# Kernel optimization log

Hardware: AMD Instinct MI355X
Metric: run time of the kernel (lower is better)

## Reference

```python
import jax, jax.numpy as jnp
import numpy as np

HID = 1024
NTOK = 16
BIAS_SCALE = 1.5
EPS = 1e-5


def layer_norm(x, g, b):
    mu = jnp.mean(x, axis=-1, keepdims=True)
    var = jnp.mean(jnp.square(x - mu), axis=-1, keepdims=True)
    return (x - mu) * jax.lax.rsqrt(var + EPS) * g + b


def setup_inputs() -> dict:
    key = jax.random.key(0)
    ks = jax.random.split(key, 16)
    B, T = 8, 4096
    Dt, Ds, Dp = 512, 512, 64
    Din = Dt + Ds + Dp

    def lin(k, fan_in, fan_out):
        bound = 1.0 / np.sqrt(fan_in)
        k1, k2 = jax.random.split(k)
        W = jax.random.uniform(k1, (fan_in, fan_out), jnp.float32, -bound, bound)
        b = jax.random.uniform(k2, (fan_out,), jnp.float32, -bound, bound)
        return W, b

    W_in, b_in = lin(ks[0], Din, HID)
    W_m1, b_m1 = lin(ks[1], HID, HID)
    W_m2, b_m2 = lin(ks[2], HID, HID)
    W_o1, b_o1 = lin(ks[3], HID, HID // 2)
    W_o2, b_o2 = lin(ks[4], HID // 2, 1)
    return {
        "trace_features": jax.random.normal(ks[5], (B, T, Dt), jnp.float32),
        "semantic_features": jax.random.normal(ks[6], (B, T, Ds), jnp.float32),
        "prior_features": jax.random.normal(ks[7], (B, T, Dp), jnp.float32),
        "W_in": W_in, "b_in": b_in,
        "ln_in_g": jnp.ones((HID,), jnp.float32), "ln_in_b": jnp.zeros((HID,), jnp.float32),
        "W_m1": W_m1, "b_m1": b_m1, "W_m2": W_m2, "b_m2": b_m2,
        "W_o1": W_o1, "b_o1": b_o1, "W_o2": W_o2, "b_o2": b_o2,
        "token_queries": jax.random.normal(ks[8], (NTOK, HID), jnp.float32) * 0.02,
        "ln_out_g": jnp.ones((HID,), jnp.float32), "ln_out_b": jnp.zeros((HID,), jnp.float32),
    }


def reference(trace_features, semantic_features, prior_features,
              W_in, b_in, ln_in_g, ln_in_b,
              W_m1, b_m1, W_m2, b_m2,
              W_o1, b_o1, W_o2, b_o2,
              token_queries, ln_out_g, ln_out_b):
    # fuse inputs: [B, T, Dt+Ds+Dp]
    fused = jnp.concatenate([trace_features, semantic_features, prior_features], axis=-1)
    h = fused @ W_in + b_in  # [B, T, H]
    mlp = jax.nn.gelu(h @ W_m1 + b_m1, approximate=False) @ W_m2 + b_m2
    seq_hidden = layer_norm(h + mlp, ln_in_g, ln_in_b)

    # objectness head -> [B, T]
    obj_logits = (jax.nn.gelu(seq_hidden @ W_o1 + b_o1, approximate=False) @ W_o2 + b_o2)[..., 0]
    objectness = jax.nn.sigmoid(obj_logits)

    # learned-query cross attention with objectness bias
    scale = float(HID) ** -0.5
    attn_logits = jnp.einsum('nh,bth->bnt', token_queries, seq_hidden) * scale
    attn_logits = attn_logits + BIAS_SCALE * objectness[:, None, :]
    attn = jax.nn.softmax(attn_logits, axis=-1)  # [B, N, T]
    token_values = jnp.einsum('bnt,bth->bnh', attn, seq_hidden)
    state_tokens = layer_norm(token_queries[None] + token_values, ln_out_g, ln_out_b)
    return state_tokens, attn, objectness
```

## Files before the change

kernel.cpp:

```cpp
#include <hip/hip_runtime.h>
#include <hip/hip_bf16.h>
#include <math.h>

typedef __bf16 bf16;
typedef __bf16 bf16x8 __attribute__((ext_vector_type(8)));
typedef __bf16 bf16x4 __attribute__((ext_vector_type(4)));
typedef float f32x4 __attribute__((ext_vector_type(4)));

#define KM 32768
#define DIN 1088

__device__ __forceinline__ void gload16(const void* g, void* l) {
  __builtin_amdgcn_global_load_lds((const __attribute__((address_space(1))) void*)g,
                                   (__attribute__((address_space(3))) void*)l, 16, 0, 0);
}

__device__ __forceinline__ float gelu_exact(float x) {
  return 0.5f * x * (1.0f + erff(x * 0.70710678118654752f));
}

__global__ void fuse_kernel(const float* __restrict__ tr, const float* __restrict__ se,
                            const float* __restrict__ pr, bf16* __restrict__ Xb) {
  int g = blockIdx.x * 256 + threadIdx.x;
  if (g >= KM * 272) return;
  int m = g / 272;
  int k0 = (g - m * 272) * 4;
  float4 v;
  if (k0 < 512)       v = *reinterpret_cast<const float4*>(tr + (size_t)m * 512 + k0);
  else if (k0 < 1024) v = *reinterpret_cast<const float4*>(se + (size_t)m * 512 + (k0 - 512));
  else                v = *reinterpret_cast<const float4*>(pr + (size_t)m * 64 + (k0 - 1024));
  union { bf16 h[4]; ushort4 u; } p;
  p.h[0] = (bf16)v.x; p.h[1] = (bf16)v.y; p.h[2] = (bf16)v.z; p.h[3] = (bf16)v.w;
  *reinterpret_cast<ushort4*>(Xb + (size_t)m * 1088 + k0) = p.u;
}

__global__ void transpose_kernel(const float* __restrict__ W, bf16* __restrict__ Wt,
                                 int K, int N) {
  __shared__ float t[32][33];
  int k0 = blockIdx.x * 32, n0 = blockIdx.y * 32;
  int tx = threadIdx.x & 31, ty = threadIdx.x >> 5;
  #pragma unroll
  for (int j = 0; j < 32; j += 8) t[ty + j][tx] = W[(size_t)(k0 + ty + j) * N + n0 + tx];
  __syncthreads();
  #pragma unroll
  for (int j = 0; j < 32; j += 8)
    Wt[(size_t)(n0 + ty + j) * K + k0 + tx] = (bf16)t[tx][ty + j];
}

template<int ACT, bool RES>
__global__ void gemm_kernel(const bf16* __restrict__ A, const bf16* __restrict__ Bt,
                            const float* __restrict__ bias, const bf16* __restrict__ res,
                            bf16* __restrict__ C, int N, int K, int nbn) {
  __shared__ __align__(16) bf16 lds[2][128 * 64];
  int bid = blockIdx.x;
  int bn = bid % nbn, bm = bid / nbn;
  int tid = threadIdx.x;
  int w = tid >> 6, L = tid & 63;
  int wm = w >> 1, wn = w & 1;
  int srow = L >> 3;
  int scol = 8 * ((L & 7) ^ srow);
  const bf16* Ab = A + (size_t)(bm * 128) * K;
  const bf16* Bb = Bt + (size_t)(bn * 128) * K;
  f32x4 acc[4][4] = {};
  int nkt = K >> 6;
  for (int kt = 0; kt < nkt; ++kt) {
    int k0 = kt << 6;
    #pragma unroll
    for (int i = 0; i < 4; ++i) {
      int row = w * 32 + i * 8;
      gload16(Ab + (size_t)(row + srow) * K + k0 + scol, &lds[0][row * 64]);
      gload16(Bb + (size_t)(row + srow) * K + k0 + scol, &lds[1][row * 64]);
    }
    __syncthreads();
    #pragma unroll
    for (int kk = 0; kk < 2; ++kk) {
      bf16x8 af[4], bfr[4];
      int cb = kk * 64 + ((L >> 4) * 16);
      #pragma unroll
      for (int m = 0; m < 4; ++m) {
        int r = wm * 64 + m * 16 + (L & 15);
        int addr = r * 128 + (cb ^ ((r & 7) << 4));
        af[m] = *reinterpret_cast<const bf16x8*>(
            reinterpret_cast<const char*>(&lds[0][0]) + addr);
      }
      #pragma unroll
      for (int n = 0; n < 4; ++n) {
        int r = wn * 64 + n * 16 + (L & 15);
        int addr = r * 128 + (cb ^ ((r & 7) << 4));
        bfr[n] = *reinterpret_cast<const bf16x8*>(
            reinterpret_cast<const char*>(&lds[1][0]) + addr);
      }
      #pragma unroll
      for (int m = 0; m < 4; ++m)
        #pragma unroll
        for (int n = 0; n < 4; ++n)
          acc[m][n] = __builtin_amdgcn_mfma_f32_16x16x32_bf16(af[m], bfr[n], acc[m][n], 0, 0, 0);
    }
    __syncthreads();
  }
  int cn0 = bn * 128 + wn * 64;
  float bv[4];
  #pragma unroll
  for (int n = 0; n < 4; ++n) bv[n] = bias[cn0 + n * 16 + (L & 15)];
  #pragma unroll
  for (int m = 0; m < 4; ++m) {
    int grow0 = bm * 128 + wm * 64 + m * 16 + ((L >> 4) << 2);
    #pragma unroll
    for (int r = 0; r < 4; ++r) {
      size_t ro = (size_t)(grow0 + r) * N;
      #pragma unroll
      for (int n = 0; n < 4; ++n) {
        float v = acc[m][n][r] + bv[n];
        if (ACT == 1) v = gelu_exact(v);
        int col = cn0 + n * 16 + (L & 15);
        if (RES) v += (float)res[ro + col];
        C[ro + col] = (bf16)v;
      }
    }
  }
}

__global__ void ln_inplace_kernel(bf16* __restrict__ X, const float* __restrict__ g,
                                  const float* __restrict__ b) {
  __shared__ float sb[4];
  size_t row = blockIdx.x;
  bf16* xr = X + row * 1024;
  int tid = threadIdx.x;
  bf16x4 xv = *reinterpret_cast<const bf16x4*>(xr + tid * 4);
  float x[4];
  #pragma unroll
  for (int i = 0; i < 4; ++i) x[i] = (float)xv[i];
  float s = x[0] + x[1] + x[2] + x[3];
  #pragma unroll
  for (int off = 32; off > 0; off >>= 1) s += __shfl_xor(s, off);
  if ((tid & 63) == 0) sb[tid >> 6] = s;
  __syncthreads();
  float mu = (sb[0] + sb[1] + sb[2] + sb[3]) * (1.0f / 1024.0f);
  __syncthreads();
  float d[4], sq = 0.f;
  #pragma unroll
  for (int i = 0; i < 4; ++i) { d[i] = x[i] - mu; sq += d[i] * d[i]; }
  #pragma unroll
  for (int off = 32; off > 0; off >>= 1) sq += __shfl_xor(sq, off);
  if ((tid & 63) == 0) sb[tid >> 6] = sq;
  __syncthreads();
  float var = (sb[0] + sb[1] + sb[2] + sb[3]) * (1.0f / 1024.0f);
  float rs = rsqrtf(var + 1e-5f);
  bf16x4 ov;
  #pragma unroll
  for (int i = 0; i < 4; ++i) ov[i] = (bf16)(d[i] * rs * g[tid * 4 + i] + b[tid * 4 + i]);
  *reinterpret_cast<bf16x4*>(xr + tid * 4) = ov;
}

__global__ void obj_kernel(const bf16* __restrict__ o1, const float* __restrict__ W2,
                           const float* __restrict__ b2, float* __restrict__ obj,
                           float* __restrict__ out_obj) {
  __shared__ float w[512];
  int tid = threadIdx.x;
  w[tid] = W2[tid]; w[tid + 256] = W2[tid + 256];
  __syncthreads();
  int wv = tid >> 6, L = tid & 63;
  size_t m = (size_t)blockIdx.x * 4 + wv;
  bf16x8 v = *reinterpret_cast<const bf16x8*>(o1 + m * 512 + L * 8);
  float s = 0.f;
  #pragma unroll
  for (int j = 0; j < 8; ++j) s += (float)v[j] * w[L * 8 + j];
  #pragma unroll
  for (int off = 32; off > 0; off >>= 1) s += __shfl_xor(s, off);
  if (L == 0) {
    float o = 1.0f / (1.0f + expf(-(s + b2[0])));
    obj[m] = o; out_obj[m] = o;
  }
}

__global__ void attn_logits_mfma(const bf16* __restrict__ seq, const float* __restrict__ tq,
                                 const float* __restrict__ obj, float* __restrict__ logits) {
  __shared__ bf16 tqs[16][1032];
  int tid = threadIdx.x;
  for (int i = tid; i < 4096; i += 256) {
    int idx = i * 4;
    int n = idx >> 10, k = idx & 1023;
    float4 v = *reinterpret_cast<const float4*>(tq + idx);
    bf16x4 p; p[0] = (bf16)v.x; p[1] = (bf16)v.y; p[2] = (bf16)v.z; p[3] = (bf16)v.w;
    *reinterpret_cast<bf16x4*>(&tqs[n][k]) = p;
  }
  __syncthreads();
  int w = tid >> 6, L = tid & 63;
  int row0 = blockIdx.x * 128 + w * 32;
  const bf16* A0 = seq + (size_t)(row0 + (L & 15)) * 1024 + ((L >> 4) * 8);
  const bf16* Bq = &tqs[L & 15][(L >> 4) * 8];
  f32x4 acc0 = {}, acc1 = {};
  #pragma unroll 4
  for (int kt = 0; kt < 32; ++kt) {
    int k0 = kt * 32;
    bf16x8 bq = *reinterpret_cast<const bf16x8*>(Bq + k0);
    bf16x8 a0 = *reinterpret_cast<const bf16x8*>(A0 + k0);
    bf16x8 a1 = *reinterpret_cast<const bf16x8*>(A0 + 16 * 1024 + k0);
    acc0 = __builtin_amdgcn_mfma_f32_16x16x32_bf16(a0, bq, acc0, 0, 0, 0);
    acc1 = __builtin_amdgcn_mfma_f32_16x16x32_bf16(a1, bq, acc1, 0, 0, 0);
  }
  int b = row0 >> 12;
  int n = L & 15;
  float* outn = logits + ((size_t)(b * 16) + n) * 4096;
  #pragma unroll
  for (int mf = 0; mf < 2; ++mf) {
    int mrow = row0 + mf * 16 + ((L >> 4) << 2);
    #pragma unroll
    for (int r = 0; r < 4; ++r) {
      int m = mrow + r;
      float v = (mf == 0 ? acc0[r] : acc1[r]) * 0.03125f + 1.5f * obj[m];
      outn[m & 4095] = v;
    }
  }
}

__global__ void softmax_kernel(const float* __restrict__ logits, float* __restrict__ attn) {
  __shared__ float sb[4];
  size_t row = blockIdx.x;
  const float* lr = logits + row * 4096;
  float* orow = attn + row * 4096;
  int tid = threadIdx.x;
  float x[16];
  #pragma unroll
  for (int i = 0; i < 4; ++i) {
    float4 v = *reinterpret_cast<const float4*>(lr + tid * 16 + i * 4);
    x[i * 4 + 0] = v.x; x[i * 4 + 1] = v.y; x[i * 4 + 2] = v.z; x[i * 4 + 3] = v.w;
  }
  float mx = -1e30f;
  #pragma unroll
  for (int j = 0; j < 16; ++j) mx = fmaxf(mx, x[j]);
  #pragma unroll
  for (int off = 32; off > 0; off >>= 1) mx = fmaxf(mx, __shfl_xor(mx, off));
  if ((tid & 63) == 0) sb[tid >> 6] = mx;
  __syncthreads();
  mx = fmaxf(fmaxf(sb[0], sb[1]), fmaxf(sb[2], sb[3]));
  __syncthreads();
  float s = 0.f;
  #pragma unroll
  for (int j = 0; j < 16; ++j) { x[j] = expf(x[j] - mx); s += x[j]; }
  #pragma unroll
  for (int off = 32; off > 0; off >>= 1) s += __shfl_xor(s, off);
  if ((tid & 63) == 0) sb[tid >> 6] = s;
  __syncthreads();
  float inv = 1.0f / (sb[0] + sb[1] + sb[2] + sb[3]);
  #pragma unroll
  for (int i = 0; i < 4; ++i) {
    float4 v = make_float4(x[i * 4] * inv, x[i * 4 + 1] * inv, x[i * 4 + 2] * inv, x[i * 4 + 3] * inv);
    *reinterpret_cast<float4*>(orow + tid * 16 + i * 4) = v;
  }
}

__global__ void token_values_kernel(const float* __restrict__ attn, const bf16* __restrict__ seq,
                                    float* __restrict__ tvp) {
  int bid = blockIdx.x;
  int split = bid & 3;
  int hc = (bid >> 2) & 15;
  int b = bid >> 6;
  __shared__ float al[16][256];
  int h = hc * 64 + (threadIdx.x & 63);
  int grp = threadIdx.x >> 6;
  float acc[4] = {0.f, 0.f, 0.f, 0.f};
  for (int c = 0; c < 4; ++c) {
    int t0 = split * 1024 + c * 256;
    __syncthreads();
    for (int i = threadIdx.x; i < 4096; i += 256)
      al[i >> 8][i & 255] = attn[((size_t)b * 16 + (i >> 8)) * 4096 + t0 + (i & 255)];
    __syncthreads();
    for (int tt = 0; tt < 256; ++tt) {
      float s = (float)seq[((size_t)b * 4096 + t0 + tt) * 1024 + h];
      #pragma unroll
      for (int i = 0; i < 4; ++i) acc[i] += al[grp * 4 + i][tt] * s;
    }
  }
  #pragma unroll
  for (int i = 0; i < 4; ++i)
    tvp[(size_t)split * 131072 + ((size_t)b * 16 + grp * 4 + i) * 1024 + h] = acc[i];
}

__global__ void final_ln_kernel(const float* __restrict__ tq, const float* __restrict__ tvp,
                                const float* __restrict__ g, const float* __restrict__ bb,
                                float* __restrict__ out0) {
  __shared__ float sb[4];
  int row = blockIdx.x;
  int n = row & 15;
  int tid = threadIdx.x;
  float x[4];
  #pragma unroll
  for (int i = 0; i < 4; ++i) {
    int h = tid * 4 + i;
    float v = tq[n * 1024 + h];
    #pragma unroll
    for (int p = 0; p < 4; ++p) v += tvp[(size_t)p * 131072 + (size_t)row * 1024 + h];
    x[i] = v;
  }
  float s = x[0] + x[1] + x[2] + x[3];
  #pragma unroll
  for (int off = 32; off > 0; off >>= 1) s += __shfl_xor(s, off);
  if ((tid & 63) == 0) sb[tid >> 6] = s;
  __syncthreads();
  float mu = (sb[0] + sb[1] + sb[2] + sb[3]) * (1.0f / 1024.0f);
  __syncthreads();
  float d[4], sq = 0.f;
  #pragma unroll
  for (int i = 0; i < 4; ++i) { d[i] = x[i] - mu; sq += d[i] * d[i]; }
  #pragma unroll
  for (int off = 32; off > 0; off >>= 1) sq += __shfl_xor(sq, off);
  if ((tid & 63) == 0) sb[tid >> 6] = sq;
  __syncthreads();
  float var = (sb[0] + sb[1] + sb[2] + sb[3]) * (1.0f / 1024.0f);
  float rs = rsqrtf(var + 1e-5f);
  #pragma unroll
  for (int i = 0; i < 4; ++i) {
    int h = tid * 4 + i;
    out0[(size_t)row * 1024 + h] = d[i] * rs * g[h] + bb[h];
  }
}

extern "C" void kernel_launch(void* const* d_in, const int* in_sizes, int n_in,
                              void* d_out, int out_size, void* d_ws, size_t ws_size,
                              hipStream_t stream) {
  const float* tr      = (const float*)d_in[0];
  const float* se      = (const float*)d_in[1];
  const float* pr      = (const float*)d_in[2];
  const float* W_in    = (const float*)d_in[3];
  const float* b_in    = (const float*)d_in[4];
  const float* ln_in_g = (const float*)d_in[5];
  const float* ln_in_b = (const float*)d_in[6];
  const float* W_m1    = (const float*)d_in[7];
  const float* b_m1    = (const float*)d_in[8];
  const float* W_m2    = (const float*)d_in[9];
  const float* b_m2    = (const float*)d_in[10];
  const float* W_o1    = (const float*)d_in[11];
  const float* b_o1    = (const float*)d_in[12];
  const float* W_o2    = (const float*)d_in[13];
  const float* b_o2    = (const float*)d_in[14];
  const float* tq      = (const float*)d_in[15];
  const float* ln_out_g= (const float*)d_in[16];
  const float* ln_out_b= (const float*)d_in[17];

  float* out       = (float*)d_out;
  float* out_state = out;
  float* out_attn  = out + 131072;
  float* out_obj   = out + 131072 + 524288;

  char* ws = (char*)d_ws;
  size_t off = 0;
  auto alloc = [&](size_t bytes) {
    char* p = ws + off;
    off += (bytes + 255) & ~(size_t)255;
    return p;
  };
  bf16*  Xb   = (bf16*)alloc(71303168);
  bf16*  t1   = Xb;
  bf16*  hb   = (bf16*)alloc(67108864);
  bf16*  o1   = hb;
  bf16*  sq   = (bf16*)alloc(67108864);
  bf16*  WbIn = (bf16*)alloc(2228224);
  bf16*  WbM1 = (bf16*)alloc(2097152);
  bf16*  WbM2 = (bf16*)alloc(2097152);
  bf16*  WbO1 = (bf16*)alloc(1048576);
  float* objw = (float*)alloc(131072 * 4);
  float* logw = (float*)alloc(2097152);
  float* tvp  = (float*)alloc(2097152);

  fuse_kernel<<<(KM * 272 + 255) / 256, 256, 0, stream>>>(tr, se, pr, Xb);
  transpose_kernel<<<dim3(34, 32), 256, 0, stream>>>(W_in, WbIn, 1088, 1024);
  transpose_kernel<<<dim3(32, 32), 256, 0, stream>>>(W_m1, WbM1, 1024, 1024);
  transpose_kernel<<<dim3(32, 32), 256, 0, stream>>>(W_m2, WbM2, 1024, 1024);
  transpose_kernel<<<dim3(32, 16), 256, 0, stream>>>(W_o1, WbO1, 1024, 512);

  gemm_kernel<0, false><<<256 * 8, 256, 0, stream>>>(Xb, WbIn, b_in, nullptr, hb, 1024, 1088, 8);
  gemm_kernel<1, false><<<256 * 8, 256, 0, stream>>>(hb, WbM1, b_m1, nullptr, t1, 1024, 1024, 8);
  gemm_kernel<0, true ><<<256 * 8, 256, 0, stream>>>(t1, WbM2, b_m2, hb, sq, 1024, 1024, 8);
  ln_inplace_kernel<<<32768, 256, 0, stream>>>(sq, ln_in_g, ln_in_b);
  gemm_kernel<1, false><<<256 * 4, 256, 0, stream>>>(sq, WbO1, b_o1, nullptr, o1, 512, 1024, 4);
  obj_kernel<<<8192, 256, 0, stream>>>(o1, W_o2, b_o2, objw, out_obj);
  attn_logits_mfma<<<256, 256, 0, stream>>>(sq, tq, objw, logw);
  softmax_kernel<<<128, 256, 0, stream>>>(logw, out_attn);
  token_values_kernel<<<512, 256, 0, stream>>>(out_attn, sq, tvp);
  final_ln_kernel<<<128, 256, 0, stream>>>(tq, tvp, ln_out_g, ln_out_b, out_state);
}
```

Measured before the change: 516.7 us.

## Replace 128x128 GEMM with 256x256 tile, 8-wave pipelined double-buffered kernel

```diff
diff --git a/kernel.cpp b/kernel.cpp
--- a/kernel.cpp
+++ b/kernel.cpp
@@ -9,6 +9,9 @@
 
 #define KM 32768
 #define DIN 1088
+
+#define BAR() asm volatile("s_barrier" ::: "memory")
+#define WAIT_VM2() asm volatile("s_waitcnt vmcnt(2)" ::: "memory")
 
 __device__ __forceinline__ void gload16(const void* g, void* l) {
   __builtin_amdgcn_global_load_lds((const __attribute__((address_space(1))) void*)g,
@@ -48,71 +51,140 @@
 }
 
 template<int ACT, bool RES>
-__global__ void gemm_kernel(const bf16* __restrict__ A, const bf16* __restrict__ Bt,
-                            const float* __restrict__ bias, const bf16* __restrict__ res,
-                            bf16* __restrict__ C, int N, int K, int nbn) {
-  __shared__ __align__(16) bf16 lds[2][128 * 64];
+__global__ __launch_bounds__(512, 2) void gemm256_kernel(
+    const bf16* __restrict__ A, const bf16* __restrict__ Bt,
+    const float* __restrict__ bias, const bf16* __restrict__ res,
+    bf16* __restrict__ C, int N, int K, int nbn) {
+  __shared__ __align__(16) bf16 ldsA[2][16384];
+  __shared__ __align__(16) bf16 ldsB[2][16384];
+  int nwg = gridDim.x;
   int bid = blockIdx.x;
-  int bn = bid % nbn, bm = bid / nbn;
+  int nb = (bid & 7) * (nwg >> 3) + (bid >> 3);
+  int bn = nb % nbn, bm = nb / nbn;
   int tid = threadIdx.x;
   int w = tid >> 6, L = tid & 63;
-  int wm = w >> 1, wn = w & 1;
-  int srow = L >> 3;
-  int scol = 8 * ((L & 7) ^ srow);
-  const bf16* Ab = A + (size_t)(bm * 128) * K;
-  const bf16* Bb = Bt + (size_t)(bn * 128) * K;
-  f32x4 acc[4][4] = {};
+  int wm = w >> 2, wn = w & 3;
+  const bf16* Ab = A + (size_t)bm * 256 * K;
+  const bf16* Bb = Bt + (size_t)bn * 256 * K;
   int nkt = K >> 6;
-  for (int kt = 0; kt < nkt; ++kt) {
-    int k0 = kt << 6;
-    #pragma unroll
-    for (int i = 0; i < 4; ++i) {
-      int row = w * 32 + i * 8;
-      gload16(Ab + (size_t)(row + srow) * K + k0 + scol, &lds[0][row * 64]);
-      gload16(Bb + (size_t)(row + srow) * K + k0 + scol, &lds[1][row * 64]);
+  int H = nkt << 2;
+
+  int lr = L >> 3;
+  int ce = ((L & 7) ^ lr) << 3;
+  auto stage = [&](int h) {
+    if (h >= H) return;
+    int tt = h >> 2, i = h & 3, bb = tt & 1;
+    int k0 = tt << 6;
+    #pragma unroll
+    for (int j = 0; j < 2; ++j) {
+      int rr = w * 16 + j * 8;
+      if (i < 2)
+        gload16(Ab + (size_t)(i * 128 + rr + lr) * K + k0 + ce, &ldsA[bb][(i * 128 + rr) * 64]);
+      else
+        gload16(Bb + (size_t)((i - 2) * 128 + rr + lr) * K + k0 + ce, &ldsB[bb][((i - 2) * 128 + rr) * 64]);
     }
-    __syncthreads();
-    #pragma unroll
-    for (int kk = 0; kk < 2; ++kk) {
-      bf16x8 af[4], bfr[4];
-      int cb = kk * 64 + ((L >> 4) * 16);
-      #pragma unroll
-      for (int m = 0; m < 4; ++m) {
-        int r = wm * 64 + m * 16 + (L & 15);
-        int addr = r * 128 + (cb ^ ((r & 7) << 4));
-        af[m] = *reinterpret_cast<const bf16x8*>(
-            reinterpret_cast<const char*>(&lds[0][0]) + addr);
-      }
-      #pragma unroll
-      for (int n = 0; n < 4; ++n) {
-        int r = wn * 64 + n * 16 + (L & 15);
-        int addr = r * 128 + (cb ^ ((r & 7) << 4));
-        bfr[n] = *reinterpret_cast<const bf16x8*>(
-            reinterpret_cast<const char*>(&lds[1][0]) + addr);
-      }
-      #pragma unroll
-      for (int m = 0; m < 4; ++m)
+  };
+  auto lread = [&](const bf16* base, int mrow, int kk) -> bf16x8 {
+    int cb = ((kk << 6) + ((L >> 4) << 4)) ^ ((L & 7) << 4);
+    return *reinterpret_cast<const bf16x8*>(
+        reinterpret_cast<const char*>(base) + (mrow + (L & 15)) * 128 + cb);
+  };
+
+  f32x4 acc[8][4] = {};
+  bf16x8 af[4][2], bq[4][2];
+
+  #pragma unroll
+  for (int h = 0; h < 5; ++h) stage(h);
+  WAIT_VM2();
+  BAR();
+
+  for (int t = 0; t < nkt; ++t) {
+    int b = t & 1;
+    const bf16* As = ldsA[b];
+    const bf16* Bs = ldsB[b];
+    #pragma unroll
+    for (int mf = 0; mf < 4; ++mf)
+      #pragma unroll
+      for (int kk = 0; kk < 2; ++kk) af[mf][kk] = lread(As, wm * 128 + mf * 16, kk);
+    #pragma unroll
+    for (int nf = 0; nf < 2; ++nf)
+      #pragma unroll
+      for (int kk = 0; kk < 2; ++kk) bq[nf][kk] = lread(Bs, wn * 64 + nf * 16, kk);
+    stage(4 * t + 5);
+    BAR();
+    __builtin_amdgcn_s_setprio(1);
+    #pragma unroll
+    for (int mf = 0; mf < 4; ++mf)
+      #pragma unroll
+      for (int nf = 0; nf < 2; ++nf)
         #pragma unroll
-        for (int n = 0; n < 4; ++n)
-          acc[m][n] = __builtin_amdgcn_mfma_f32_16x16x32_bf16(af[m], bfr[n], acc[m][n], 0, 0, 0);
-    }
-    __syncthreads();
-  }
-  int cn0 = bn * 128 + wn * 64;
+        for (int kk = 0; kk < 2; ++kk)
+          acc[mf][nf] = __builtin_amdgcn_mfma_f32_16x16x32_bf16(af[mf][kk], bq[nf][kk], acc[mf][nf], 0, 0, 0);
+    __builtin_amdgcn_s_setprio(0);
+    BAR();
+    #pragma unroll
+    for (int nf = 2; nf < 4; ++nf)
+      #pragma unroll
+      for (int kk = 0; kk < 2; ++kk) bq[nf][kk] = lread(Bs, wn * 64 + nf * 16, kk);
+    stage(4 * t + 6);
+    BAR();
+    __builtin_amdgcn_s_setprio(1);
+    #pragma unroll
+    for (int mf = 0; mf < 4; ++mf)
+      #pragma unroll
+      for (int nf = 2; nf < 4; ++nf)
+        #pragma unroll
+        for (int kk = 0; kk < 2; ++kk)
+          acc[mf][nf] = __builtin_amdgcn_mfma_f32_16x16x32_bf16(af[mf][kk], bq[nf][kk], acc[mf][nf], 0, 0, 0);
+    __builtin_amdgcn_s_setprio(0);
+    BAR();
+    #pragma unroll
+    for (int mf = 0; mf < 4; ++mf)
+      #pragma unroll
+      for (int kk = 0; kk < 2; ++kk) af[mf][kk] = lread(As, wm * 128 + 64 + mf * 16, kk);
+    stage(4 * t + 7);
+    BAR();
+    __builtin_amdgcn_s_setprio(1);
+    #pragma unroll
+    for (int mf = 0; mf < 4; ++mf)
+      #pragma unroll
+      for (int nf = 0; nf < 2; ++nf)
+        #pragma unroll
+        for (int kk = 0; kk < 2; ++kk)
+          acc[4 + mf][nf] = __builtin_amdgcn_mfma_f32_16x16x32_bf16(af[mf][kk], bq[nf][kk], acc[4 + mf][nf], 0, 0, 0);
+    __builtin_amdgcn_s_setprio(0);
+    BAR();
+    stage(4 * t + 8);
+    WAIT_VM2();
+    BAR();
+    __builtin_amdgcn_s_setprio(1);
+    #pragma unroll
+    for (int mf = 0; mf < 4; ++mf)
+      #pragma unroll
+      for (int nf = 2; nf < 4; ++nf)
+        #pragma unroll
+        for (int kk = 0; kk < 2; ++kk)
+          acc[4 + mf][nf] = __builtin_amdgcn_mfma_f32_16x16x32_bf16(af[mf][kk], bq[nf][kk], acc[4 + mf][nf], 0, 0, 0);
+    __builtin_amdgcn_s_setprio(0);
+    BAR();
+  }
+
+  int row0 = bm * 256 + wm * 128;
+  int col0 = bn * 256 + wn * 64;
   float bv[4];
   #pragma unroll
-  for (int n = 0; n < 4; ++n) bv[n] = bias[cn0 + n * 16 + (L & 15)];
-  #pragma unroll
-  for (int m = 0; m < 4; ++m) {
-    int grow0 = bm * 128 + wm * 64 + m * 16 + ((L >> 4) << 2);
-    #pragma unroll
-    for (int r = 0; r < 4; ++r) {
-      size_t ro = (size_t)(grow0 + r) * N;
-      #pragma unroll
-      for (int n = 0; n < 4; ++n) {
-        float v = acc[m][n][r] + bv[n];
+  for (int nf = 0; nf < 4; ++nf) bv[nf] = bias[col0 + nf * 16 + (L & 15)];
+  #pragma unroll
+  for (int mf = 0; mf < 8; ++mf) {
+    int grow = row0 + mf * 16 + ((L >> 4) << 2);
+    #pragma unroll
+    for (int rr = 0; rr < 4; ++rr) {
+      size_t ro = (size_t)(grow + rr) * N;
+      #pragma unroll
+      for (int nf = 0; nf < 4; ++nf) {
+        float v = acc[mf][nf][rr] + bv[nf];
         if (ACT == 1) v = gelu_exact(v);
-        int col = cn0 + n * 16 + (L & 15);
+        int col = col0 + nf * 16 + (L & 15);
         if (RES) v += (float)res[ro + col];
         C[ro + col] = (bf16)v;
       }
@@ -369,11 +441,11 @@
   transpose_kernel<<<dim3(32, 32), 256, 0, stream>>>(W_m2, WbM2, 1024, 1024);
   transpose_kernel<<<dim3(32, 16), 256, 0, stream>>>(W_o1, WbO1, 1024, 512);
 
-  gemm_kernel<0, false><<<256 * 8, 256, 0, stream>>>(Xb, WbIn, b_in, nullptr, hb, 1024, 1088, 8);
-  gemm_kernel<1, false><<<256 * 8, 256, 0, stream>>>(hb, WbM1, b_m1, nullptr, t1, 1024, 1024, 8);
-  gemm_kernel<0, true ><<<256 * 8, 256, 0, stream>>>(t1, WbM2, b_m2, hb, sq, 1024, 1024, 8);
+  gemm256_kernel<0, false><<<512, 512, 0, stream>>>(Xb, WbIn, b_in, nullptr, hb, 1024, 1088, 4);
+  gemm256_kernel<1, false><<<512, 512, 0, stream>>>(hb, WbM1, b_m1, nullptr, t1, 1024, 1024, 4);
+  gemm256_kernel<0, true ><<<512, 512, 0, stream>>>(t1, WbM2, b_m2, hb, sq, 1024, 1024, 4);
   ln_inplace_kernel<<<32768, 256, 0, stream>>>(sq, ln_in_g, ln_in_b);
-  gemm_kernel<1, false><<<256 * 4, 256, 0, stream>>>(sq, WbO1, b_o1, nullptr, o1, 512, 1024, 4);
+  gemm256_kernel<1, false><<<256, 512, 0, stream>>>(sq, WbO1, b_o1, nullptr, o1, 512, 1024, 2);
   obj_kernel<<<8192, 256, 0, stream>>>(o1, W_o2, b_o2, objw, out_obj);
   attn_logits_mfma<<<256, 256, 0, stream>>>(sq, tq, objw, logw);
   softmax_kernel<<<128, 256, 0, stream>>>(logw, out_attn);
```

New measurement: 496.5 us. -3.9%, faster.
